# Kernel optimization log

Hardware: AMD Instinct MI355X
Metric: run time of the kernel (lower is better)

Reference implementation:

```python
import jax, jax.numpy as jnp
import numpy as np

MAXLEN = 100  # target_node_incoming_edge_maxlim in to_dense_batch_JY


def setup_inputs() -> dict:
    key = jax.random.key(0)
    ks = jax.random.split(key, 6)
    N, F, H, B = 500000, 64, 64, 8192
    x = jax.random.normal(ks[0], (N, F), dtype=jnp.float32)
    index = jnp.sort(jax.random.randint(ks[1], (N,), 0, B)).astype(jnp.int64)
    s = 1.0 / np.sqrt(H)  # torch LSTM reset_parameters: U(-1/sqrt(H), 1/sqrt(H))
    W_ih = jax.random.uniform(ks[2], (4 * H, F), jnp.float32, -s, s)
    W_hh = jax.random.uniform(ks[3], (4 * H, H), jnp.float32, -s, s)
    b_ih = jax.random.uniform(ks[4], (4 * H,), jnp.float32, -s, s)
    b_hh = jax.random.uniform(ks[5], (4 * H,), jnp.float32, -s, s)
    return {"x": x, "W_ih": W_ih, "W_hh": W_hh, "b_ih": b_ih, "b_hh": b_hh,
            "index": index, "dim_size": B}


def _lstm_last_hidden(dense, mask, W_ih, W_hh, b_ih, b_hh):
    """Run a single-layer LSTM over dense [B,L,F]; freeze state where mask is
    False, which reproduces pack_sequence semantics (ht = hidden at last valid
    step of each sequence; zero-length sequences stay at h0=0)."""
    B, L, F = dense.shape
    H = W_hh.shape[1]
    # input projection for all timesteps at once: [B, L, 4H]
    xg = jnp.einsum('blf,gf->blg', dense, W_ih) + (b_ih + b_hh)

    def step(carry, inp):
        h, c = carry
        g_x, m = inp                      # g_x: [B,4H], m: [B] bool
        g = g_x + h @ W_hh.T
        i, f, gc, o = jnp.split(g, 4, axis=-1)  # torch gate order: i, f, g, o
        i = jax.nn.sigmoid(i)
        f = jax.nn.sigmoid(f)
        gc = jnp.tanh(gc)
        o = jax.nn.sigmoid(o)
        c_new = f * c + i * gc
        h_new = o * jnp.tanh(c_new)
        m2 = m[:, None]
        return (jnp.where(m2, h_new, h), jnp.where(m2, c_new, c)), None

    h0 = jnp.zeros((B, H), dense.dtype)
    (h, _c), _ = jax.lax.scan(step, (h0, h0),
                              (jnp.swapaxes(xg, 0, 1), mask.T))
    return h  # [B, H] == ht[-1]


def reference(x, W_ih, W_hh, b_ih, b_hh, index, dim_size):
    N, F = x.shape
    index = index.astype(jnp.int32)
    # per-graph node counts and exclusive-cumsum offsets (index is sorted)
    counts = jax.ops.segment_sum(jnp.ones(N, jnp.int32), index,
                                 num_segments=dim_size)
    offsets = jnp.concatenate([jnp.zeros(1, jnp.int32),
                               jnp.cumsum(counts)[:-1].astype(jnp.int32)])
    pos = jnp.arange(N, dtype=jnp.int32) - offsets[index]  # position in graph
    valid = pos < MAXLEN                                   # truncate to 100
    # scatter into dense [B, MAXLEN, F]; invalid rows are zeroed and added at
    # slot 0 so they are no-ops
    dense = jnp.zeros((dim_size, MAXLEN, F), x.dtype)
    dense = dense.at[index, jnp.where(valid, pos, 0)].add(
        jnp.where(valid[:, None], x, 0.0))
    seq_len = jnp.minimum(counts, MAXLEN)
    mask = jnp.arange(MAXLEN)[None, :] < seq_len[:, None]  # [B, MAXLEN]
    return _lstm_last_hidden(dense, mask, W_ih, W_hh, b_ih, b_hh)
```

## Files before the change

### kernel.cpp

```cpp
#include <hip/hip_runtime.h>

#define MAXLEN 100
#define HDIM 64
#define CH 8
#define SROW 72
#define SPLANE (CH * SROW + 8)
#define HSTR 72
#define L2E 1.44269504f

typedef __attribute__((ext_vector_type(8))) short bf16x8;
typedef __attribute__((ext_vector_type(4))) float f32x4;

__device__ __forceinline__ unsigned short f2bf_u(float f) {
    unsigned u = __float_as_uint(f);
    u += 0x7fffu + ((u >> 16) & 1u);
    return (unsigned short)(u >> 16);
}
__device__ __forceinline__ unsigned pk2(float a, float b) {
    return (unsigned)f2bf_u(a) | ((unsigned)f2bf_u(b) << 16);
}
__device__ __forceinline__ bf16x8 pack8(f32x4 a, f32x4 b) {
    union { unsigned u[4]; bf16x8 v; } c;
    c.u[0] = pk2(a[0], a[1]); c.u[1] = pk2(a[2], a[3]);
    c.u[2] = pk2(b[0], b[1]); c.u[3] = pk2(b[2], b[3]);
    return c.v;
}
__device__ __forceinline__ float sig_b(float v, float bs) {
    return __builtin_amdgcn_rcpf(1.0f + __builtin_amdgcn_exp2f(fmaf(v, -L2E, bs)));
}
__device__ __forceinline__ float tanh_b(float v, float bs2) {
    return fmaf(2.0f, __builtin_amdgcn_rcpf(1.0f + __builtin_amdgcn_exp2f(fmaf(v, -2.0f * L2E, bs2))), -1.0f);
}
__device__ __forceinline__ float tanh_p(float v) {
    return fmaf(2.0f, __builtin_amdgcn_rcpf(1.0f + __builtin_amdgcn_exp2f(v * (-2.0f * L2E))), -1.0f);
}

__global__ __launch_bounds__(256, 4)
void lstm8_kernel(const float* __restrict__ x,
                  const float* __restrict__ Wih,
                  const float* __restrict__ Whh,
                  const float* __restrict__ bih,
                  const float* __restrict__ bhh,
                  const int* __restrict__ index,
                  float* __restrict__ out, int N, int B) {
    const int tid  = threadIdx.x;
    const int w    = tid >> 6;
    const int lane = tid & 63;
    const int l15  = lane & 15;
    const int quad = lane >> 4;
    const int segbase = blockIdx.x * 8;
    const int ncol = w * 16 + l15;

    __shared__ __align__(16) unsigned short xst[9 * SPLANE];
    __shared__ __align__(16) unsigned short hst[2][16][HSTR];
    __shared__ int sstart[8], slen[8];

    if (tid < 8) {
        const int b = segbase + tid;
        int s = 0, len = 0;
        if (b < B) {
            int lo = 0, hi = N;
            while (lo < hi) { int m = (lo + hi) >> 1; if (index[m] < b) lo = m + 1; else hi = m; }
            s = lo;
            hi = N;
            while (lo < hi) { int m = (lo + hi) >> 1; if (index[m] < b + 1) lo = m + 1; else hi = m; }
            len = lo - s;
            len = len < MAXLEN ? len : MAXLEN;
        }
        sstart[tid] = s;
        slen[tid] = len;
    }
    for (int i = tid; i < 2 * 16 * HSTR / 2; i += 256) ((int*)hst)[i] = 0;
    for (int i = tid; i < SPLANE / 2; i += 256) ((int*)xst)[8 * SPLANE / 2 + i] = 0;
    __syncthreads();

    bf16x8 wi[4][2], wh[4][2];
    float bs[4];
#pragma unroll
    for (int g = 0; g < 4; ++g) {
        const int row = g * HDIM + ncol;
        const float bb = bih[row] + bhh[row];
        bs[g] = (g == 2) ? (-2.0f * L2E) * bb : (-L2E) * bb;
#pragma unroll
        for (int kt = 0; kt < 2; ++kt) {
            const f32x4* pi = (const f32x4*)(Wih + (size_t)row * HDIM + kt * 32 + quad * 8);
            const f32x4* ph = (const f32x4*)(Whh + (size_t)row * HDIM + kt * 32 + quad * 8);
            wi[g][kt] = pack8(pi[0], pi[1]);
            wh[g][kt] = pack8(ph[0], ph[1]);
        }
    }

    int len2[2];
    len2[0] = slen[2 * quad];
    len2[1] = slen[2 * quad + 1];
    int lmax = 0;
#pragma unroll
    for (int i = 0; i < 8; ++i) { int v = slen[i]; lmax = v > lmax ? v : lmax; }

    const int sS = tid >> 5, sT = (tid >> 2) & 7, sC = tid & 3;
    const int sst = sstart[sS], sln = slen[sS];

    f32x4 pre[4];

#define ISSUE(t0_)                                                              \
    {                                                                           \
        int rr = (t0_) + sT;                                                    \
        rr = (sln > 0) ? (rr < sln ? rr : sln - 1) : 0;                         \
        long long row = (long long)sst + rr;                                    \
        row = row < (long long)(N - 1) ? row : (long long)(N - 1);              \
        const f32x4* p_ = (const f32x4*)(x + row * HDIM + sC * 16);             \
        pre[0] = p_[0]; pre[1] = p_[1]; pre[2] = p_[2]; pre[3] = p_[3];         \
    }
#define COMMIT()                                                                \
    {                                                                           \
        uint4 o1, o2;                                                           \
        o1.x = pk2(pre[0][0], pre[0][1]); o1.y = pk2(pre[0][2], pre[0][3]);     \
        o1.z = pk2(pre[1][0], pre[1][1]); o1.w = pk2(pre[1][2], pre[1][3]);     \
        o2.x = pk2(pre[2][0], pre[2][1]); o2.y = pk2(pre[2][2], pre[2][3]);     \
        o2.z = pk2(pre[3][0], pre[3][1]); o2.w = pk2(pre[3][2], pre[3][3]);     \
        unsigned short* d_ = &xst[sS * SPLANE + sT * SROW + sC * 16];           \
        *(uint4*)d_ = o1; *(uint4*)(d_ + 8) = o2;                               \
    }

    const int xp = (l15 & 2) ? 8 : ((l15 >> 2) * 2 + (l15 & 1));
    const unsigned short* xb = &xst[xp * SPLANE + quad * 8];

    float c2[2] = {0, 0}, h2[2] = {0, 0};
    const f32x4 cz = {0.0f, 0.0f, 0.0f, 0.0f};
    const int nch = (lmax + CH - 1) / CH;

    if (nch > 0) {
        ISSUE(0);
        COMMIT();
        __syncthreads();
        ISSUE(CH);

        for (int ch = 0; ch < nch; ++ch) {
            const int t0 = ch * CH;
#pragma unroll
            for (int tt = 0; tt < CH; ++tt) {
                const int t = t0 + tt;
                const int pb = tt & 1, nb = pb ^ 1;

                const unsigned short* xr = xb + tt * SROW;
                bf16x8 xa0 = *(const bf16x8*)(xr);
                bf16x8 xa1 = *(const bf16x8*)(xr + 32);
                const unsigned short* hr = &hst[pb][l15][quad * 8];
                bf16x8 ha0 = *(const bf16x8*)(hr);
                bf16x8 ha1 = *(const bf16x8*)(hr + 32);

                f32x4 acc[4];
#pragma unroll
                for (int g = 0; g < 4; ++g) {
                    f32x4 a = __builtin_amdgcn_mfma_f32_16x16x32_bf16(xa0, wi[g][0], cz, 0, 0, 0);
                    a = __builtin_amdgcn_mfma_f32_16x16x32_bf16(xa1, wi[g][1], a, 0, 0, 0);
                    a = __builtin_amdgcn_mfma_f32_16x16x32_bf16(ha0, wh[g][0], a, 0, 0, 0);
                    a = __builtin_amdgcn_mfma_f32_16x16x32_bf16(ha1, wh[g][1], a, 0, 0, 0);
                    acc[g] = a;
                }

#pragma unroll
                for (int r = 0; r < 2; ++r) {
                    float gi = sig_b (acc[0][r], bs[0]);
                    float gf = sig_b (acc[1][r], bs[1]);
                    float gg = tanh_b(acc[2][r], bs[2]);
                    float go = sig_b (acc[3][r], bs[3]);
                    float cn = fmaf(gf, c2[r], gi * gg);
                    float hn = go * tanh_p(cn);
                    const bool up = t < len2[r];
                    c2[r] = up ? cn : c2[r];
                    h2[r] = up ? hn : h2[r];
                    hst[nb][quad * 4 + r][ncol] = f2bf_u(h2[r]);
                }
                __syncthreads();
            }
            if (ch + 1 < nch) {
                COMMIT();
                __syncthreads();
                ISSUE((ch + 2) * CH);
            }
        }
    }

#pragma unroll
    for (int r = 0; r < 2; ++r) {
        const int seg = segbase + 2 * quad + r;
        if (seg < B) out[(size_t)seg * HDIM + ncol] = h2[r];
    }
#undef ISSUE
#undef COMMIT
}

extern "C" void kernel_launch(void* const* d_in, const int* in_sizes, int n_in,
                              void* d_out, int out_size, void* d_ws, size_t ws_size,
                              hipStream_t stream) {
    const float* x     = (const float*)d_in[0];
    const float* Wih   = (const float*)d_in[1];
    const float* Whh   = (const float*)d_in[2];
    const float* bih   = (const float*)d_in[3];
    const float* bhh   = (const float*)d_in[4];
    const int*   index = (const int*)d_in[5];

    const int N = in_sizes[5];
    const int B = out_size / HDIM;

    const int nblocks = (B + 7) / 8;
    lstm8_kernel<<<nblocks, 256, 0, stream>>>(x, Wih, Whh, bih, bhh, index,
                                              (float*)d_out, N, B);
}
```

Measured before the change: 257.2 us.

## Prefetch x chunks via global_load_lds DMA and use lgkm-only barriers

Replaces the register-staged prefetch of x rows with direct global-to-LDS DMA loads (global_load_lds) into a new fp32 staging buffer, then converts to bf16 in LDS after waiting on vmcnt. Per-step __syncthreads are replaced by an inline-asm lgkmcnt(0)+s_barrier so the outstanding DMA loads are not waited on at every timestep. It aims to free prefetch registers and let global loads overlap the recurrent steps, at the cost of 16KB extra LDS, which may reduce occupancy, and reliance on manual waitcnt correctness.

```diff
diff --git a/kernel.cpp b/kernel.cpp
--- a/kernel.cpp
+++ b/kernel.cpp
@@ -10,6 +10,15 @@
 
 typedef __attribute__((ext_vector_type(8))) short bf16x8;
 typedef __attribute__((ext_vector_type(4))) float f32x4;
+typedef unsigned int u32;
+
+#define LGKM_BARRIER() asm volatile("s_waitcnt lgkmcnt(0)\n\ts_barrier" ::: "memory")
+#define WAIT_VM0()     asm volatile("s_waitcnt vmcnt(0)" ::: "memory")
+
+__device__ __forceinline__ void dma16(const float* g, u32* lds) {
+    __builtin_amdgcn_global_load_lds((const __attribute__((address_space(1))) u32*)g,
+                                     (__attribute__((address_space(3))) u32*)lds, 16, 0, 0);
+}
 
 __device__ __forceinline__ unsigned short f2bf_u(float f) {
     unsigned u = __float_as_uint(f);
@@ -51,24 +60,21 @@
     const int segbase = blockIdx.x * 8;
     const int ncol = w * 16 + l15;
 
+    __shared__ __align__(16) float xf32[8 * CH * HDIM];
     __shared__ __align__(16) unsigned short xst[9 * SPLANE];
     __shared__ __align__(16) unsigned short hst[2][16][HSTR];
     __shared__ int sstart[8], slen[8];
 
     if (tid < 8) {
         const int b = segbase + tid;
-        int s = 0, len = 0;
-        if (b < B) {
-            int lo = 0, hi = N;
-            while (lo < hi) { int m = (lo + hi) >> 1; if (index[m] < b) lo = m + 1; else hi = m; }
-            s = lo;
-            hi = N;
-            while (lo < hi) { int m = (lo + hi) >> 1; if (index[m] < b + 1) lo = m + 1; else hi = m; }
-            len = lo - s;
-            len = len < MAXLEN ? len : MAXLEN;
-        }
+        int lo = 0, hi = N;
+        while (lo < hi) { int m = (lo + hi) >> 1; if (index[m] < b) lo = m + 1; else hi = m; }
+        const int s = lo;
+        hi = N;
+        while (lo < hi) { int m = (lo + hi) >> 1; if (index[m] < b + 1) lo = m + 1; else hi = m; }
+        int len = lo - s;
         sstart[tid] = s;
-        slen[tid] = len;
+        slen[tid] = len < MAXLEN ? len : MAXLEN;
     }
     for (int i = tid; i < 2 * 16 * HSTR / 2; i += 256) ((int*)hst)[i] = 0;
     for (int i = tid; i < SPLANE / 2; i += 256) ((int*)xst)[8 * SPLANE / 2 + i] = 0;
@@ -97,29 +103,45 @@
 #pragma unroll
     for (int i = 0; i < 8; ++i) { int v = slen[i]; lmax = v > lmax ? v : lmax; }
 
-    const int sS = tid >> 5, sT = (tid >> 2) & 7, sC = tid & 3;
-    const int sst = sstart[sS], sln = slen[sS];
-
-    f32x4 pre[4];
-
-#define ISSUE(t0_)                                                              \
-    {                                                                           \
-        int rr = (t0_) + sT;                                                    \
-        rr = (sln > 0) ? (rr < sln ? rr : sln - 1) : 0;                         \
-        long long row = (long long)sst + rr;                                    \
-        row = row < (long long)(N - 1) ? row : (long long)(N - 1);              \
-        const f32x4* p_ = (const f32x4*)(x + row * HDIM + sC * 16);             \
-        pre[0] = p_[0]; pre[1] = p_[1]; pre[2] = p_[2]; pre[3] = p_[3];         \
-    }
-#define COMMIT()                                                                \
-    {                                                                           \
-        uint4 o1, o2;                                                           \
-        o1.x = pk2(pre[0][0], pre[0][1]); o1.y = pk2(pre[0][2], pre[0][3]);     \
-        o1.z = pk2(pre[1][0], pre[1][1]); o1.w = pk2(pre[1][2], pre[1][3]);     \
-        o2.x = pk2(pre[2][0], pre[2][1]); o2.y = pk2(pre[2][2], pre[2][3]);     \
-        o2.z = pk2(pre[3][0], pre[3][1]); o2.w = pk2(pre[3][2], pre[3][3]);     \
-        unsigned short* d_ = &xst[sS * SPLANE + sT * SROW + sC * 16];           \
-        *(uint4*)d_ = o1; *(uint4*)(d_ + 8) = o2;                               \
+    const int s0 = 2 * w, s1 = 2 * w + 1;
+    const int st0 = sstart[s0], st1 = sstart[s1];
+    const int sl0 = slen[s0],   sl1 = slen[s1];
+    const int lrow = lane >> 4, lcol = (lane & 15) * 4;
+
+#define CLAMPT(t_, sl_) ((sl_) > 0 ? ((t_) < (sl_) ? (t_) : (sl_) - 1) : 0)
+#define CROW(st_, ct_)  ({ long long r_ = (long long)(st_) + (ct_);              \
+                           r_ > (long long)(N - 1) ? (long long)(N - 1) : r_; })
+#define DMA(t0_)                                                                 \
+    {                                                                            \
+        const int ta = (t0_) + lrow;                                             \
+        long long rA0 = CROW(st0, CLAMPT(ta,     sl0));                          \
+        long long rA1 = CROW(st0, CLAMPT(ta + 4, sl0));                          \
+        long long rB0 = CROW(st1, CLAMPT(ta,     sl1));                          \
+        long long rB1 = CROW(st1, CLAMPT(ta + 4, sl1));                          \
+        dma16(x + rA0 * HDIM + lcol, (u32*)&xf32[s0 * CH * HDIM]);               \
+        dma16(x + rA1 * HDIM + lcol, (u32*)&xf32[s0 * CH * HDIM + 4 * HDIM]);    \
+        dma16(x + rB0 * HDIM + lcol, (u32*)&xf32[s1 * CH * HDIM]);               \
+        dma16(x + rB1 * HDIM + lcol, (u32*)&xf32[s1 * CH * HDIM + 4 * HDIM]);    \
+    }
+
+    const int cseg = 2 * w + (lane >> 5);
+    const int crow = (lane >> 2) & 7;
+    const int ccol = (lane & 3) * 16;
+    const float* csrc = &xf32[(cseg * CH + crow) * HDIM + ccol];
+    unsigned short* cdst = &xst[cseg * SPLANE + crow * SROW + ccol];
+
+#define CONVERT()                                                                \
+    {                                                                            \
+        f32x4 a0 = *(const f32x4*)csrc;                                          \
+        f32x4 a1 = *(const f32x4*)(csrc + 4);                                    \
+        f32x4 a2 = *(const f32x4*)(csrc + 8);                                    \
+        f32x4 a3 = *(const f32x4*)(csrc + 12);                                   \
+        uint4 o1, o2;                                                            \
+        o1.x = pk2(a0[0], a0[1]); o1.y = pk2(a0[2], a0[3]);                      \
+        o1.z = pk2(a1[0], a1[1]); o1.w = pk2(a1[2], a1[3]);                      \
+        o2.x = pk2(a2[0], a2[1]); o2.y = pk2(a2[2], a2[3]);                      \
+        o2.z = pk2(a3[0], a3[1]); o2.w = pk2(a3[2], a3[3]);                      \
+        *(uint4*)cdst = o1; *(uint4*)(cdst + 8) = o2;                            \
     }
 
     const int xp = (l15 & 2) ? 8 : ((l15 >> 2) * 2 + (l15 & 1));
@@ -130,10 +152,11 @@
     const int nch = (lmax + CH - 1) / CH;
 
     if (nch > 0) {
-        ISSUE(0);
-        COMMIT();
-        __syncthreads();
-        ISSUE(CH);
+        DMA(0);
+        WAIT_VM0();
+        CONVERT();
+        LGKM_BARRIER();
+        if (nch > 1) DMA(CH);
 
         for (int ch = 0; ch < nch; ++ch) {
             const int t0 = ch * CH;
@@ -172,12 +195,13 @@
                     h2[r] = up ? hn : h2[r];
                     hst[nb][quad * 4 + r][ncol] = f2bf_u(h2[r]);
                 }
-                __syncthreads();
+                LGKM_BARRIER();
             }
             if (ch + 1 < nch) {
-                COMMIT();
-                __syncthreads();
-                ISSUE((ch + 2) * CH);
+                WAIT_VM0();
+                CONVERT();
+                LGKM_BARRIER();
+                if (ch + 2 < nch) DMA((ch + 2) * CH);
             }
         }
     }
@@ -187,8 +211,10 @@
         const int seg = segbase + 2 * quad + r;
         if (seg < B) out[(size_t)seg * HDIM + ncol] = h2[r];
     }
-#undef ISSUE
-#undef COMMIT
+#undef DMA
+#undef CONVERT
+#undef CLAMPT
+#undef CROW
 }
 
 extern "C" void kernel_launch(void* const* d_in, const int* in_sizes, int n_in,
```

After: 270.4 us. +5.1%, slower.

## Shrink x staging chunk to 4 steps and use lightweight LDS barriers

Applied to the files above, without the earlier changes.

Halves the per-chunk x prefetch (CH 8→4) so each thread loads two float4s instead of four, cutting register pressure. __syncthreads is replaced by an inline s_waitcnt lgkmcnt(0) + s_barrier, which does not wait on outstanding global loads, so the prefetched x rows can stay in flight across the timestep barriers. Gate MFMAs are reordered so the sigmoid/tanh for one gate pair can overlap the MFMAs of the next, redundant prefetches past the last chunk are skipped, and lmax is made wave-uniform. The cost is twice as many chunk commits and extra barriers, and the inline asm barrier relies on no vmcnt dependency across it.

```diff
diff --git a/kernel.cpp b/kernel.cpp
--- a/kernel.cpp
+++ b/kernel.cpp
@@ -2,7 +2,7 @@
 
 #define MAXLEN 100
 #define HDIM 64
-#define CH 8
+#define CH 4
 #define SROW 72
 #define SPLANE (CH * SROW + 8)
 #define HSTR 72
@@ -10,6 +10,8 @@
 
 typedef __attribute__((ext_vector_type(8))) short bf16x8;
 typedef __attribute__((ext_vector_type(4))) float f32x4;
+
+#define LGKM_BARRIER() asm volatile("s_waitcnt lgkmcnt(0)\n\ts_barrier" ::: "memory")
 
 __device__ __forceinline__ unsigned short f2bf_u(float f) {
     unsigned u = __float_as_uint(f);
@@ -96,30 +98,28 @@
     int lmax = 0;
 #pragma unroll
     for (int i = 0; i < 8; ++i) { int v = slen[i]; lmax = v > lmax ? v : lmax; }
-
-    const int sS = tid >> 5, sT = (tid >> 2) & 7, sC = tid & 3;
+    lmax = __builtin_amdgcn_readfirstlane(lmax);
+
+    const int sS = tid >> 5, sT = (tid >> 3) & 3, sC = tid & 7;
     const int sst = sstart[sS], sln = slen[sS];
 
-    f32x4 pre[4];
+    f32x4 pre0, pre1;
 
 #define ISSUE(t0_)                                                              \
     {                                                                           \
-        int rr = (t0_) + sT;                                                    \
-        rr = (sln > 0) ? (rr < sln ? rr : sln - 1) : 0;                         \
-        long long row = (long long)sst + rr;                                    \
-        row = row < (long long)(N - 1) ? row : (long long)(N - 1);              \
-        const f32x4* p_ = (const f32x4*)(x + row * HDIM + sC * 16);             \
-        pre[0] = p_[0]; pre[1] = p_[1]; pre[2] = p_[2]; pre[3] = p_[3];         \
+        int ct = (t0_) + sT;                                                    \
+        ct = (sln > 0) ? (ct < sln ? ct : sln - 1) : 0;                         \
+        int row = sst + ct;                                                     \
+        row = row < N - 1 ? row : N - 1;                                        \
+        const f32x4* p_ = (const f32x4*)(x + (size_t)row * HDIM + sC * 8);      \
+        pre0 = p_[0]; pre1 = p_[1];                                             \
     }
 #define COMMIT()                                                                \
     {                                                                           \
-        uint4 o1, o2;                                                           \
-        o1.x = pk2(pre[0][0], pre[0][1]); o1.y = pk2(pre[0][2], pre[0][3]);     \
-        o1.z = pk2(pre[1][0], pre[1][1]); o1.w = pk2(pre[1][2], pre[1][3]);     \
-        o2.x = pk2(pre[2][0], pre[2][1]); o2.y = pk2(pre[2][2], pre[2][3]);     \
-        o2.z = pk2(pre[3][0], pre[3][1]); o2.w = pk2(pre[3][2], pre[3][3]);     \
-        unsigned short* d_ = &xst[sS * SPLANE + sT * SROW + sC * 16];           \
-        *(uint4*)d_ = o1; *(uint4*)(d_ + 8) = o2;                               \
+        uint4 o_;                                                               \
+        o_.x = pk2(pre0[0], pre0[1]); o_.y = pk2(pre0[2], pre0[3]);             \
+        o_.z = pk2(pre1[0], pre1[1]); o_.w = pk2(pre1[2], pre1[3]);             \
+        *(uint4*)&xst[sS * SPLANE + sT * SROW + sC * 8] = o_;                   \
     }
 
     const int xp = (l15 & 2) ? 8 : ((l15 >> 2) * 2 + (l15 & 1));
@@ -132,8 +132,8 @@
     if (nch > 0) {
         ISSUE(0);
         COMMIT();
-        __syncthreads();
-        ISSUE(CH);
+        LGKM_BARRIER();
+        if (nch > 1) ISSUE(CH);
 
         for (int ch = 0; ch < nch; ++ch) {
             const int t0 = ch * CH;
@@ -149,35 +149,54 @@
                 bf16x8 ha0 = *(const bf16x8*)(hr);
                 bf16x8 ha1 = *(const bf16x8*)(hr + 32);
 
-                f32x4 acc[4];
-#pragma unroll
-                for (int g = 0; g < 4; ++g) {
-                    f32x4 a = __builtin_amdgcn_mfma_f32_16x16x32_bf16(xa0, wi[g][0], cz, 0, 0, 0);
-                    a = __builtin_amdgcn_mfma_f32_16x16x32_bf16(xa1, wi[g][1], a, 0, 0, 0);
-                    a = __builtin_amdgcn_mfma_f32_16x16x32_bf16(ha0, wh[g][0], a, 0, 0, 0);
-                    a = __builtin_amdgcn_mfma_f32_16x16x32_bf16(ha1, wh[g][1], a, 0, 0, 0);
-                    acc[g] = a;
-                }
-
-#pragma unroll
-                for (int r = 0; r < 2; ++r) {
-                    float gi = sig_b (acc[0][r], bs[0]);
-                    float gf = sig_b (acc[1][r], bs[1]);
-                    float gg = tanh_b(acc[2][r], bs[2]);
-                    float go = sig_b (acc[3][r], bs[3]);
-                    float cn = fmaf(gf, c2[r], gi * gg);
-                    float hn = go * tanh_p(cn);
-                    const bool up = t < len2[r];
-                    c2[r] = up ? cn : c2[r];
-                    h2[r] = up ? hn : h2[r];
-                    hst[nb][quad * 4 + r][ncol] = f2bf_u(h2[r]);
-                }
-                __syncthreads();
+                float gi0, gi1, gf0, gf1, gg0, gg1, go0, go1;
+                {
+                    f32x4 a0 = __builtin_amdgcn_mfma_f32_16x16x32_bf16(xa0, wi[0][0], cz, 0, 0, 0);
+                    a0 = __builtin_amdgcn_mfma_f32_16x16x32_bf16(xa1, wi[0][1], a0, 0, 0, 0);
+                    a0 = __builtin_amdgcn_mfma_f32_16x16x32_bf16(ha0, wh[0][0], a0, 0, 0, 0);
+                    a0 = __builtin_amdgcn_mfma_f32_16x16x32_bf16(ha1, wh[0][1], a0, 0, 0, 0);
+                    f32x4 a1 = __builtin_amdgcn_mfma_f32_16x16x32_bf16(xa0, wi[1][0], cz, 0, 0, 0);
+                    a1 = __builtin_amdgcn_mfma_f32_16x16x32_bf16(xa1, wi[1][1], a1, 0, 0, 0);
+                    a1 = __builtin_amdgcn_mfma_f32_16x16x32_bf16(ha0, wh[1][0], a1, 0, 0, 0);
+                    a1 = __builtin_amdgcn_mfma_f32_16x16x32_bf16(ha1, wh[1][1], a1, 0, 0, 0);
+                    gi0 = sig_b(a0[0], bs[0]); gi1 = sig_b(a0[1], bs[0]);
+                    gf0 = sig_b(a1[0], bs[1]); gf1 = sig_b(a1[1], bs[1]);
+                }
+                {
+                    f32x4 a2 = __builtin_amdgcn_mfma_f32_16x16x32_bf16(xa0, wi[2][0], cz, 0, 0, 0);
+                    a2 = __builtin_amdgcn_mfma_f32_16x16x32_bf16(xa1, wi[2][1], a2, 0, 0, 0);
+                    a2 = __builtin_amdgcn_mfma_f32_16x16x32_bf16(ha0, wh[2][0], a2, 0, 0, 0);
+                    a2 = __builtin_amdgcn_mfma_f32_16x16x32_bf16(ha1, wh[2][1], a2, 0, 0, 0);
+                    f32x4 a3 = __builtin_amdgcn_mfma_f32_16x16x32_bf16(xa0, wi[3][0], cz, 0, 0, 0);
+                    a3 = __builtin_amdgcn_mfma_f32_16x16x32_bf16(xa1, wi[3][1], a3, 0, 0, 0);
+                    a3 = __builtin_amdgcn_mfma_f32_16x16x32_bf16(ha0, wh[3][0], a3, 0, 0, 0);
+                    a3 = __builtin_amdgcn_mfma_f32_16x16x32_bf16(ha1, wh[3][1], a3, 0, 0, 0);
+                    gg0 = tanh_b(a2[0], bs[2]); gg1 = tanh_b(a2[1], bs[2]);
+                    go0 = sig_b (a3[0], bs[3]); go1 = sig_b (a3[1], bs[3]);
+                }
+
+                {
+                    float cn = fmaf(gf0, c2[0], gi0 * gg0);
+                    float hn = go0 * tanh_p(cn);
+                    const bool up = t < len2[0];
+                    c2[0] = up ? cn : c2[0];
+                    h2[0] = up ? hn : h2[0];
+                    hst[nb][quad * 4 + 0][ncol] = f2bf_u(h2[0]);
+                }
+                {
+                    float cn = fmaf(gf1, c2[1], gi1 * gg1);
+                    float hn = go1 * tanh_p(cn);
+                    const bool up = t < len2[1];
+                    c2[1] = up ? cn : c2[1];
+                    h2[1] = up ? hn : h2[1];
+                    hst[nb][quad * 4 + 1][ncol] = f2bf_u(h2[1]);
+                }
+                LGKM_BARRIER();
             }
             if (ch + 1 < nch) {
                 COMMIT();
-                __syncthreads();
-                ISSUE((ch + 2) * CH);
+                LGKM_BARRIER();
+                if (ch + 2 < nch) ISSUE((ch + 2) * CH);
             }
         }
     }
```

Measured after the change: 264.2 us. 2.7% more time.

## Pack twelve sequences per block using three MFMA rows per quad

Applied to the files above, without the earlier changes.

Each block now processes 12 sequences instead of 8, filling 3 of the 4 accumulator rows per quad rather than 2, so the per-step MFMA and barrier cost is spread over more sequences and fewer blocks are launched. The x staging loads are remapped to three 32-byte loads per thread over 12 sequence planes. __syncthreads is replaced with an explicit lgkmcnt wait plus s_barrier, and a redundant prefetch past the last chunk is skipped. Occupancy is lowered to 3 blocks per CU, and the longest sequence in a block of 12 sets how many chunks that block runs, which may add wasted steps.

```diff
diff --git a/kernel.cpp b/kernel.cpp
--- a/kernel.cpp
+++ b/kernel.cpp
@@ -3,6 +3,7 @@
 #define MAXLEN 100
 #define HDIM 64
 #define CH 8
+#define NSEG 12
 #define SROW 72
 #define SPLANE (CH * SROW + 8)
 #define HSTR 72
@@ -10,6 +11,8 @@
 
 typedef __attribute__((ext_vector_type(8))) short bf16x8;
 typedef __attribute__((ext_vector_type(4))) float f32x4;
+
+#define LGKM_BARRIER() asm volatile("s_waitcnt lgkmcnt(0)\n\ts_barrier" ::: "memory")
 
 __device__ __forceinline__ unsigned short f2bf_u(float f) {
     unsigned u = __float_as_uint(f);
@@ -35,27 +38,27 @@
     return fmaf(2.0f, __builtin_amdgcn_rcpf(1.0f + __builtin_amdgcn_exp2f(v * (-2.0f * L2E))), -1.0f);
 }
 
-__global__ __launch_bounds__(256, 4)
-void lstm8_kernel(const float* __restrict__ x,
-                  const float* __restrict__ Wih,
-                  const float* __restrict__ Whh,
-                  const float* __restrict__ bih,
-                  const float* __restrict__ bhh,
-                  const int* __restrict__ index,
-                  float* __restrict__ out, int N, int B) {
+__global__ __launch_bounds__(256, 3)
+void lstm12_kernel(const float* __restrict__ x,
+                   const float* __restrict__ Wih,
+                   const float* __restrict__ Whh,
+                   const float* __restrict__ bih,
+                   const float* __restrict__ bhh,
+                   const int* __restrict__ index,
+                   float* __restrict__ out, int N, int B) {
     const int tid  = threadIdx.x;
     const int w    = tid >> 6;
     const int lane = tid & 63;
     const int l15  = lane & 15;
     const int quad = lane >> 4;
-    const int segbase = blockIdx.x * 8;
+    const int segbase = blockIdx.x * NSEG;
     const int ncol = w * 16 + l15;
 
-    __shared__ __align__(16) unsigned short xst[9 * SPLANE];
+    __shared__ __align__(16) unsigned short xst[NSEG * SPLANE];
     __shared__ __align__(16) unsigned short hst[2][16][HSTR];
-    __shared__ int sstart[8], slen[8];
-
-    if (tid < 8) {
+    __shared__ int sstart[NSEG], slen[NSEG];
+
+    if (tid < NSEG) {
         const int b = segbase + tid;
         int s = 0, len = 0;
         if (b < B) {
@@ -71,7 +74,6 @@
         slen[tid] = len;
     }
     for (int i = tid; i < 2 * 16 * HSTR / 2; i += 256) ((int*)hst)[i] = 0;
-    for (int i = tid; i < SPLANE / 2; i += 256) ((int*)xst)[8 * SPLANE / 2 + i] = 0;
     __syncthreads();
 
     bf16x8 wi[4][2], wh[4][2];
@@ -90,50 +92,60 @@
         }
     }
 
-    int len2[2];
-    len2[0] = slen[2 * quad];
-    len2[1] = slen[2 * quad + 1];
+    int len3[3];
+#pragma unroll
+    for (int r = 0; r < 3; ++r) len3[r] = slen[quad * 3 + r];
     int lmax = 0;
 #pragma unroll
-    for (int i = 0; i < 8; ++i) { int v = slen[i]; lmax = v > lmax ? v : lmax; }
-
-    const int sS = tid >> 5, sT = (tid >> 2) & 7, sC = tid & 3;
-    const int sst = sstart[sS], sln = slen[sS];
-
-    f32x4 pre[4];
+    for (int i = 0; i < NSEG; ++i) { int v = slen[i]; lmax = v > lmax ? v : lmax; }
+    lmax = __builtin_amdgcn_readfirstlane(lmax);
+
+    const int ustep = (tid >> 3) & 7, ugrp = tid & 7;
+    const int us0 = tid >> 6;
+    int sst3[3], sln3[3];
+#pragma unroll
+    for (int k = 0; k < 3; ++k) { sst3[k] = sstart[us0 + 4 * k]; sln3[k] = slen[us0 + 4 * k]; }
+
+    f32x4 pre[3][2];
 
 #define ISSUE(t0_)                                                              \
     {                                                                           \
-        int rr = (t0_) + sT;                                                    \
-        rr = (sln > 0) ? (rr < sln ? rr : sln - 1) : 0;                         \
-        long long row = (long long)sst + rr;                                    \
-        row = row < (long long)(N - 1) ? row : (long long)(N - 1);              \
-        const f32x4* p_ = (const f32x4*)(x + row * HDIM + sC * 16);             \
-        pre[0] = p_[0]; pre[1] = p_[1]; pre[2] = p_[2]; pre[3] = p_[3];         \
+        _Pragma("unroll")                                                       \
+        for (int k_ = 0; k_ < 3; ++k_) {                                        \
+            int ct = (t0_) + ustep;                                             \
+            ct = (sln3[k_] > 0) ? (ct < sln3[k_] ? ct : sln3[k_] - 1) : 0;      \
+            int row = sst3[k_] + ct;                                            \
+            row = row < N - 1 ? row : N - 1;                                    \
+            const f32x4* p_ = (const f32x4*)(x + (size_t)row * HDIM + ugrp * 8);\
+            pre[k_][0] = p_[0]; pre[k_][1] = p_[1];                             \
+        }                                                                       \
     }
 #define COMMIT()                                                                \
     {                                                                           \
-        uint4 o1, o2;                                                           \
-        o1.x = pk2(pre[0][0], pre[0][1]); o1.y = pk2(pre[0][2], pre[0][3]);     \
-        o1.z = pk2(pre[1][0], pre[1][1]); o1.w = pk2(pre[1][2], pre[1][3]);     \
-        o2.x = pk2(pre[2][0], pre[2][1]); o2.y = pk2(pre[2][2], pre[2][3]);     \
-        o2.z = pk2(pre[3][0], pre[3][1]); o2.w = pk2(pre[3][2], pre[3][3]);     \
-        unsigned short* d_ = &xst[sS * SPLANE + sT * SROW + sC * 16];           \
-        *(uint4*)d_ = o1; *(uint4*)(d_ + 8) = o2;                               \
-    }
-
-    const int xp = (l15 & 2) ? 8 : ((l15 >> 2) * 2 + (l15 & 1));
+        _Pragma("unroll")                                                       \
+        for (int k_ = 0; k_ < 3; ++k_) {                                        \
+            uint4 o_;                                                           \
+            o_.x = pk2(pre[k_][0][0], pre[k_][0][1]);                           \
+            o_.y = pk2(pre[k_][0][2], pre[k_][0][3]);                           \
+            o_.z = pk2(pre[k_][1][0], pre[k_][1][1]);                           \
+            o_.w = pk2(pre[k_][1][2], pre[k_][1][3]);                           \
+            *(uint4*)&xst[(us0 + 4 * k_) * SPLANE + ustep * SROW + ugrp * 8] = o_; \
+        }                                                                       \
+    }
+
+    const int m3 = l15 & 3;
+    const int xp = (l15 >> 2) * 3 + (m3 < 2 ? m3 : 2);
     const unsigned short* xb = &xst[xp * SPLANE + quad * 8];
 
-    float c2[2] = {0, 0}, h2[2] = {0, 0};
+    float c3[3] = {0, 0, 0}, h3[3] = {0, 0, 0};
     const f32x4 cz = {0.0f, 0.0f, 0.0f, 0.0f};
     const int nch = (lmax + CH - 1) / CH;
 
     if (nch > 0) {
         ISSUE(0);
         COMMIT();
-        __syncthreads();
-        ISSUE(CH);
+        LGKM_BARRIER();
+        if (nch > 1) ISSUE(CH);
 
         for (int ch = 0; ch < nch; ++ch) {
             const int t0 = ch * CH;
@@ -160,32 +172,32 @@
                 }
 
 #pragma unroll
-                for (int r = 0; r < 2; ++r) {
+                for (int r = 0; r < 3; ++r) {
                     float gi = sig_b (acc[0][r], bs[0]);
                     float gf = sig_b (acc[1][r], bs[1]);
                     float gg = tanh_b(acc[2][r], bs[2]);
                     float go = sig_b (acc[3][r], bs[3]);
-                    float cn = fmaf(gf, c2[r], gi * gg);
+                    float cn = fmaf(gf, c3[r], gi * gg);
                     float hn = go * tanh_p(cn);
-                    const bool up = t < len2[r];
-                    c2[r] = up ? cn : c2[r];
-                    h2[r] = up ? hn : h2[r];
-                    hst[nb][quad * 4 + r][ncol] = f2bf_u(h2[r]);
+                    const bool up = t < len3[r];
+                    c3[r] = up ? cn : c3[r];
+                    h3[r] = up ? hn : h3[r];
+                    hst[nb][quad * 4 + r][ncol] = f2bf_u(h3[r]);
                 }
-                __syncthreads();
+                LGKM_BARRIER();
             }
             if (ch + 1 < nch) {
                 COMMIT();
-                __syncthreads();
-                ISSUE((ch + 2) * CH);
+                LGKM_BARRIER();
+                if (ch + 2 < nch) ISSUE((ch + 2) * CH);
             }
         }
     }
 
 #pragma unroll
-    for (int r = 0; r < 2; ++r) {
-        const int seg = segbase + 2 * quad + r;
-        if (seg < B) out[(size_t)seg * HDIM + ncol] = h2[r];
+    for (int r = 0; r < 3; ++r) {
+        const int seg = segbase + quad * 3 + r;
+        if (seg < B) out[(size_t)seg * HDIM + ncol] = h3[r];
     }
 #undef ISSUE
 #undef COMMIT
@@ -204,7 +216,7 @@
     const int N = in_sizes[5];
     const int B = out_size / HDIM;
 
-    const int nblocks = (B + 7) / 8;
-    lstm8_kernel<<<nblocks, 256, 0, stream>>>(x, Wih, Whh, bih, bhh, index,
-                                              (float*)d_out, N, B);
-}
+    const int nblocks = (B + NSEG - 1) / NSEG;
+    lstm12_kernel<<<nblocks, 256, 0, stream>>>(x, Wih, Whh, bih, bhh, index,
+                                               (float*)d_out, N, B);
+}
```

New measurement: 258.5 us. About the same (+0.5%).
